# Performance work log

Hardware: AMD Instinct MI355X
Metric: run time of the kernel (lower is better)

## Reference

```python
import jax, jax.numpy as jnp
import numpy as np
from jax import lax

K = 15            # contrast_kernel
BRIGHT_T = 0.7    # brightness_threshold

def _box_filter(x, k):
    # x: [B,1,H,W]; uniform k x k conv with SAME (zero) padding, matching F.conv2d(padding=k//2)
    kernel = jnp.full((1, 1, k, k), 1.0 / (k * k), dtype=x.dtype)
    pad = k // 2
    return lax.conv_general_dilated(
        x, kernel, window_strides=(1, 1), padding=[(pad, pad), (pad, pad)],
        dimension_numbers=('NCHW', 'OIHW', 'NCHW'))

def _avg_pool_5x5(x):
    # avg_pool2d(kernel=5, stride=1, padding=2), count_include_pad=True (torch default)
    s = lax.reduce_window(x, jnp.array(0.0, x.dtype), lax.add,
                          window_dimensions=(1, 1, 5, 5), window_strides=(1, 1, 1, 1),
                          padding=[(0, 0), (0, 0), (2, 2), (2, 2)])
    return s / jnp.array(25.0, x.dtype)

def setup_inputs() -> dict:
    key = jax.random.key(0)
    img = jax.random.uniform(key, (16, 3, 1024, 1024), dtype=jnp.float32)
    return {"img": img}

def reference(img) -> jnp.ndarray:
    # luminance: [B,1,H,W]
    lum = (0.299 * img[:, 0:1] + 0.587 * img[:, 1:2] + 0.114 * img[:, 2:3])
    brightness_mask = jax.nn.sigmoid((lum - BRIGHT_T) * 10.0)
    local_mean = _box_filter(lum, K)
    local_var = _box_filter((lum - local_mean) ** 2, K)
    contrast_mask = jax.nn.sigmoid(local_var * 50.0 - 0.5)
    max_rgb = jnp.max(img, axis=1, keepdims=True)
    min_rgb = jnp.min(img, axis=1, keepdims=True)
    saturation = (max_rgb - min_rgb) / (max_rgb + 1e-8)
    low_sat_mask = jax.nn.sigmoid((0.3 - saturation) * 10.0)
    combined = jnp.clip(brightness_mask + 0.5 * contrast_mask * low_sat_mask, 0.0, 1.0)
    return _avg_pool_5x5(combined)
```

## Files before the change

### kernel.cpp

```cpp
#include <hip/hip_runtime.h>


#define BLOCK 512
typedef unsigned short u16;
typedef unsigned int u32;
typedef __attribute__((ext_vector_type(2))) float f32x2;

#define SL 104
#define S1 88

__device__ __forceinline__ float blo(u32 u){ return __uint_as_float(u << 16); }
__device__ __forceinline__ float bhi(u32 u){ return __uint_as_float(u & 0xffff0000u); }
__device__ __forceinline__ u32 pk2(float lo, float hi){
    u32 r; asm("v_cvt_pk_bf16_f32 %0, %1, %2" : "=v"(r) : "v"(lo), "v"(hi)); return r;
}
__device__ __forceinline__ f32x2 pka(f32x2 a, f32x2 b){
    f32x2 d; asm("v_pk_add_f32 %0, %1, %2" : "=v"(d) : "v"(a), "v"(b)); return d;
}
__device__ __forceinline__ f32x2 up2(u32 u){
    f32x2 r; r.x = __uint_as_float(u << 16); r.y = __uint_as_float(u & 0xffff0000u); return r;
}
__device__ __forceinline__ float sigf(float x){ return 1.f / (1.f + __expf(-x)); }
__device__ __forceinline__ float clamp01(float x){ return fminf(fmaxf(x, 0.f), 1.f); }
__device__ __forceinline__ void unp8(uint4 v, float* o){
    o[0]=blo(v.x); o[1]=bhi(v.x); o[2]=blo(v.y); o[3]=bhi(v.y);
    o[4]=blo(v.z); o[5]=bhi(v.z); o[6]=blo(v.w); o[7]=bhi(v.w);
}
__device__ __forceinline__ float satm(float r_, float g_, float b_){
    float mx = fmaxf(r_, fmaxf(g_, b_));
    float mn = fminf(r_, fminf(g_, b_));
    float sat = (mx - mn) / (mx + 1e-8f);
    return sigf((0.3f - sat) * 10.f);
}

template<bool EDGE>
__device__ __forceinline__ void body(const float* __restrict__ pR,
                                     const float* __restrict__ pG,
                                     const float* __restrict__ pB,
                                     float* __restrict__ po,
                                     int oy, int ox, int tid,
                                     u16* sLum, u16* sT1, u16* sDC)
{
    const float C225 = 1.f / 225.f;
    const float CF   = 50.f / 225.f;

    for (int task = tid; task < 96 * 6; task += BLOCK) {
        int r = task / 6, c = task - r * 6;
        int gy = oy - 16 + r;
        int gxb = ox - 16 + 16 * c;
        u32 pk[8];
        #pragma unroll
        for (int sq = 0; sq < 4; ++sq) {
            int gx = gxb + 4 * sq;
            float l0 = 0.f, l1 = 0.f, l2 = 0.f, l3 = 0.f;
            if (!EDGE || ((unsigned)gy < 1024u && (unsigned)gx < 1024u)) {
                int idx = gy * 1024 + gx;
                float4 R  = *(const float4*)&pR[idx];
                float4 G  = *(const float4*)&pG[idx];
                float4 Bc = *(const float4*)&pB[idx];
                l0 = fmaf(0.299f, R.x, fmaf(0.587f, G.x, 0.114f * Bc.x));
                l1 = fmaf(0.299f, R.y, fmaf(0.587f, G.y, 0.114f * Bc.y));
                l2 = fmaf(0.299f, R.z, fmaf(0.587f, G.z, 0.114f * Bc.z));
                l3 = fmaf(0.299f, R.w, fmaf(0.587f, G.w, 0.114f * Bc.w));
            }
            pk[2 * sq]     = pk2(l0, l1);
            pk[2 * sq + 1] = pk2(l2, l3);
        }
        u16* dst = &sLum[r * SL + 16 * c];
        *(uint4*)dst     = make_uint4(pk[0], pk[1], pk[2], pk[3]);
        *(uint4*)(dst+8) = make_uint4(pk[4], pk[5], pk[6], pk[7]);
    }
    __syncthreads();

    for (int task = tid; task < 6 * 96; task += BLOCK) {
        int g = task / 96, r = task - g * 96;
        int s0 = 16 * g;
        const u16* lr = &sLum[r * SL + s0];
        float lv[32];
        unp8(*(const uint4*)lr,        lv);
        unp8(*(const uint4*)(lr + 8),  lv + 8);
        unp8(*(const uint4*)(lr + 16), lv + 16);
        unp8(*(const uint4*)(lr + 24), lv + 24);
        float o[16];
        float s = 0.f;
        #pragma unroll
        for (int k = 0; k < 15; ++k) s += lv[k];
        o[0] = s;
        #pragma unroll
        for (int j = 1; j < 16; ++j) { s += lv[j + 14] - lv[j - 1]; o[j] = s; }
        u16* dst = &sT1[r * S1 + s0];
        if (g < 5) {
            *(uint4*)dst     = make_uint4(pk2(o[0],o[1]), pk2(o[2],o[3]),
                                          pk2(o[4],o[5]), pk2(o[6],o[7]));
            *(uint4*)(dst+8) = make_uint4(pk2(o[8],o[9]),  pk2(o[10],o[11]),
                                          pk2(o[12],o[13]),pk2(o[14],o[15]));
        } else {
            *(uint2*)dst = make_uint2(pk2(o[0],o[1]), pk2(o[2],o[3]));
        }
    }
    __syncthreads();

    for (int task = tid; task < 231; task += BLOCK) {
        int rg = task / 11, cg = task - rg * 11;
        int r0 = 4 * rg, c0 = 8 * cg;
        const u16* hp = &sT1[r0 * S1 + c0];
        f32x2 cs0, cs1, cs2, cs3;
        f32x2 n00,n01,n02,n03, n10,n11,n12,n13, n20,n21,n22,n23;
        {
            uint4 v = *(const uint4*)hp;
            cs0 = up2(v.x); cs1 = up2(v.y); cs2 = up2(v.z); cs3 = up2(v.w);
            n00 = -cs0; n01 = -cs1; n02 = -cs2; n03 = -cs3;
        }
        {
            uint4 v = *(const uint4*)(hp + S1);
            f32x2 e0 = up2(v.x), e1 = up2(v.y), e2 = up2(v.z), e3 = up2(v.w);
            n10 = -e0; n11 = -e1; n12 = -e2; n13 = -e3;
            cs0 = pka(cs0, e0); cs1 = pka(cs1, e1);
            cs2 = pka(cs2, e2); cs3 = pka(cs3, e3);
        }
        {
            uint4 v = *(const uint4*)(hp + 2 * S1);
            f32x2 e0 = up2(v.x), e1 = up2(v.y), e2 = up2(v.z), e3 = up2(v.w);
            n20 = -e0; n21 = -e1; n22 = -e2; n23 = -e3;
            cs0 = pka(cs0, e0); cs1 = pka(cs1, e1);
            cs2 = pka(cs2, e2); cs3 = pka(cs3, e3);
        }
        #pragma unroll
        for (int k = 3; k < 15; ++k) {
            uint4 v = *(const uint4*)(hp + k * S1);
            cs0 = pka(cs0, up2(v.x)); cs1 = pka(cs1, up2(v.y));
            cs2 = pka(cs2, up2(v.z)); cs3 = pka(cs3, up2(v.w));
        }
        auto emitD = [&](int row) {
            const u16* lrow = &sLum[(row + 7) * SL + c0];
            u32 aw  = *(const u32*)(lrow + 6);
            uint4 bv = *(const uint4*)(lrow + 8);
            float L0 = bhi(aw);
            float L1 = blo(bv.x), L2 = bhi(bv.x);
            float L3 = blo(bv.y), L4 = bhi(bv.y);
            float L5 = blo(bv.z), L6 = bhi(bv.z);
            float L7 = blo(bv.w);
            float t0 = fmaf(-C225, cs0.x, L0), t1 = fmaf(-C225, cs0.y, L1);
            float t2 = fmaf(-C225, cs1.x, L2), t3 = fmaf(-C225, cs1.y, L3);
            float t4 = fmaf(-C225, cs2.x, L4), t5 = fmaf(-C225, cs2.y, L5);
            float t6 = fmaf(-C225, cs3.x, L6), t7 = fmaf(-C225, cs3.y, L7);
            float d0=t0*t0, d1=t1*t1, d2=t2*t2, d3=t3*t3;
            float d4=t4*t4, d5=t5*t5, d6=t6*t6, d7=t7*t7;
            if (EDGE) {
                int gy = oy - 9 + row, gx = ox - 9 + c0;
                bool vy = (unsigned)gy < 1024u;
                d0 = (vy && (unsigned)(gx    ) < 1024u) ? d0 : 0.f;
                d1 = (vy && (unsigned)(gx + 1) < 1024u) ? d1 : 0.f;
                d2 = (vy && (unsigned)(gx + 2) < 1024u) ? d2 : 0.f;
                d3 = (vy && (unsigned)(gx + 3) < 1024u) ? d3 : 0.f;
                d4 = (vy && (unsigned)(gx + 4) < 1024u) ? d4 : 0.f;
                d5 = (vy && (unsigned)(gx + 5) < 1024u) ? d5 : 0.f;
                d6 = (vy && (unsigned)(gx + 6) < 1024u) ? d6 : 0.f;
                d7 = (vy && (unsigned)(gx + 7) < 1024u) ? d7 : 0.f;
            }
            *(uint4*)&sDC[row * S1 + c0] =
                make_uint4(pk2(d0,d1), pk2(d2,d3), pk2(d4,d5), pk2(d6,d7));
        };
        emitD(r0);
        {
            uint4 v = *(const uint4*)(hp + 15 * S1);
            cs0 = pka(pka(cs0, up2(v.x)), n00); cs1 = pka(pka(cs1, up2(v.y)), n01);
            cs2 = pka(pka(cs2, up2(v.z)), n02); cs3 = pka(pka(cs3, up2(v.w)), n03);
        }
        emitD(r0 + 1);
        {
            uint4 v = *(const uint4*)(hp + 16 * S1);
            cs0 = pka(pka(cs0, up2(v.x)), n10); cs1 = pka(pka(cs1, up2(v.y)), n11);
            cs2 = pka(pka(cs2, up2(v.z)), n12); cs3 = pka(pka(cs3, up2(v.w)), n13);
        }
        emitD(r0 + 2);
        {
            uint4 v = *(const uint4*)(hp + 17 * S1);
            cs0 = pka(pka(cs0, up2(v.x)), n20); cs1 = pka(pka(cs1, up2(v.y)), n21);
            cs2 = pka(pka(cs2, up2(v.z)), n22); cs3 = pka(pka(cs3, up2(v.w)), n23);
        }
        emitD(r0 + 3);
    }
    __syncthreads();

    for (int task = tid; task < 5 * 82; task += BLOCK) {
        int g = task / 82, r = task - g * 82;
        int s0 = 16 * g;
        const u16* dr = &sDC[r * S1 + s0];
        float lv[32];
        unp8(*(const uint4*)dr,        lv);
        unp8(*(const uint4*)(dr + 8),  lv + 8);
        unp8(*(const uint4*)(dr + 16), lv + 16);
        unp8(*(const uint4*)(dr + 24), lv + 24);
        float o[16];
        float s = 0.f;
        #pragma unroll
        for (int k = 0; k < 15; ++k) s += lv[k];
        o[0] = s;
        #pragma unroll
        for (int j = 1; j < 16; ++j) { s += lv[j + 14] - lv[j - 1]; o[j] = s; }
        u16* dst = &sT1[r * S1 + s0];
        if (g < 4) {
            *(uint4*)dst     = make_uint4(pk2(o[0],o[1]), pk2(o[2],o[3]),
                                          pk2(o[4],o[5]), pk2(o[6],o[7]));
            *(uint4*)(dst+8) = make_uint4(pk2(o[8],o[9]),  pk2(o[10],o[11]),
                                          pk2(o[12],o[13]),pk2(o[14],o[15]));
        } else {
            *(uint2*)dst = make_uint2(pk2(o[0],o[1]), pk2(o[2],o[3]));
        }
    }
    __syncthreads();

    for (int task = tid; task < 289; task += BLOCK) {
        int rg = task / 17, q = task - rg * 17;
        int r0 = 4 * rg, c0 = 4 * q;
        const u16* hp = &sT1[r0 * S1 + c0];
        f32x2 cs0, cs1, n00,n01, n10,n11, n20,n21;
        {
            uint2 v = *(const uint2*)hp;
            cs0 = up2(v.x); cs1 = up2(v.y);
            n00 = -cs0; n01 = -cs1;
        }
        {
            uint2 v = *(const uint2*)(hp + S1);
            f32x2 e0 = up2(v.x), e1 = up2(v.y);
            n10 = -e0; n11 = -e1;
            cs0 = pka(cs0, e0); cs1 = pka(cs1, e1);
        }
        {
            uint2 v = *(const uint2*)(hp + 2 * S1);
            f32x2 e0 = up2(v.x), e1 = up2(v.y);
            n20 = -e0; n21 = -e1;
            cs0 = pka(cs0, e0); cs1 = pka(cs1, e1);
        }
        #pragma unroll
        for (int k = 3; k < 15; ++k) {
            uint2 v = *(const uint2*)(hp + k * S1);
            cs0 = pka(cs0, up2(v.x)); cs1 = pka(cs1, up2(v.y));
        }
        auto emitC = [&](int row) {
            float cm0 = sigf(fmaf(cs0.x, CF, -0.5f));
            float cm1 = sigf(fmaf(cs0.y, CF, -0.5f));
            float cm2 = sigf(fmaf(cs1.x, CF, -0.5f));
            float cm3 = sigf(fmaf(cs1.y, CF, -0.5f));
            const u16* lr = &sLum[(row + 14) * SL + c0 + 14];
            u32 la = *(const u32*)lr;
            u32 lb = *(const u32*)(lr + 2);
            float bm0 = sigf((blo(la) - 0.7f) * 10.f);
            float bm1 = sigf((bhi(la) - 0.7f) * 10.f);
            float bm2 = sigf((blo(lb) - 0.7f) * 10.f);
            float bm3 = sigf((bhi(lb) - 0.7f) * 10.f);
            int gy = oy - 2 + row, gx0 = ox - 2 + c0;
            int i0 = gy * 1024 + gx0;
            float2 z2 = make_float2(0.f, 0.f);
            float2 Ra, Rb, Ga, Gb, Ba, Bb;
            bool va = true, vb = true;
            if (EDGE) {
                bool vy = (unsigned)gy < 1024u;
                va = vy && (unsigned)gx0 < 1024u;
                vb = vy && (unsigned)(gx0 + 2) < 1024u;
                Ra = va ? *(const float2*)&pR[i0]     : z2;
                Rb = vb ? *(const float2*)&pR[i0 + 2] : z2;
                Ga = va ? *(const float2*)&pG[i0]     : z2;
                Gb = vb ? *(const float2*)&pG[i0 + 2] : z2;
                Ba = va ? *(const float2*)&pB[i0]     : z2;
                Bb = vb ? *(const float2*)&pB[i0 + 2] : z2;
            } else {
                Ra = *(const float2*)&pR[i0];  Rb = *(const float2*)&pR[i0 + 2];
                Ga = *(const float2*)&pG[i0];  Gb = *(const float2*)&pG[i0 + 2];
                Ba = *(const float2*)&pB[i0];  Bb = *(const float2*)&pB[i0 + 2];
            }
            float cb0 = clamp01(bm0 + 0.5f * cm0 * satm(Ra.x, Ga.x, Ba.x));
            float cb1 = clamp01(bm1 + 0.5f * cm1 * satm(Ra.y, Ga.y, Ba.y));
            float cb2 = clamp01(bm2 + 0.5f * cm2 * satm(Rb.x, Gb.x, Bb.x));
            float cb3 = clamp01(bm3 + 0.5f * cm3 * satm(Rb.y, Gb.y, Bb.y));
            if (EDGE) {
                cb0 = va ? cb0 : 0.f;  cb1 = va ? cb1 : 0.f;
                cb2 = vb ? cb2 : 0.f;  cb3 = vb ? cb3 : 0.f;
            }
            *(uint2*)&sDC[row * S1 + c0] = make_uint2(pk2(cb0,cb1), pk2(cb2,cb3));
        };
        emitC(r0);
        {
            uint2 v = *(const uint2*)(hp + 15 * S1);
            cs0 = pka(pka(cs0, up2(v.x)), n00); cs1 = pka(pka(cs1, up2(v.y)), n01);
        }
        emitC(r0 + 1);
        {
            uint2 v = *(const uint2*)(hp + 16 * S1);
            cs0 = pka(pka(cs0, up2(v.x)), n10); cs1 = pka(pka(cs1, up2(v.y)), n11);
        }
        emitC(r0 + 2);
        {
            uint2 v = *(const uint2*)(hp + 17 * S1);
            cs0 = pka(pka(cs0, up2(v.x)), n20); cs1 = pka(pka(cs1, up2(v.y)), n21);
        }
        emitC(r0 + 3);
    }
    __syncthreads();

    for (int task = tid; task < 4 * 68; task += BLOCK) {
        int g = task / 68, r = task - g * 68;
        int s0 = 16 * g;
        const u16* cr = &sDC[r * S1 + s0];
        float cv[24];
        unp8(*(const uint4*)cr,        cv);
        unp8(*(const uint4*)(cr + 8),  cv + 8);
        unp8(*(const uint4*)(cr + 16), cv + 16);
        float o[16];
        float s = cv[0] + cv[1] + cv[2] + cv[3] + cv[4];
        o[0] = s;
        #pragma unroll
        for (int j = 1; j < 16; ++j) { s += cv[j + 4] - cv[j - 1]; o[j] = s; }
        u16* dst = &sT1[r * S1 + s0];
        *(uint4*)dst = make_uint4(pk2(o[0], o[1]), pk2(o[2], o[3]),
                                  pk2(o[4], o[5]), pk2(o[6], o[7]));
        *(uint4*)(dst + 8) = make_uint4(pk2(o[8],  o[9]),  pk2(o[10], o[11]),
                                        pk2(o[12], o[13]), pk2(o[14], o[15]));
    }
    __syncthreads();

    for (int task = tid; task < 256; task += BLOCK) {
        int rg = task >> 4, q = task & 15;
        int r0 = 4 * rg, c0 = 4 * q;
        const u16* hp = &sT1[r0 * S1 + c0];
        f32x2 cs0, cs1, n00,n01, n10,n11, n20,n21;
        {
            uint2 v = *(const uint2*)hp;
            cs0 = up2(v.x); cs1 = up2(v.y);
            n00 = -cs0; n01 = -cs1;
        }
        {
            uint2 v = *(const uint2*)(hp + S1);
            f32x2 e0 = up2(v.x), e1 = up2(v.y);
            n10 = -e0; n11 = -e1;
            cs0 = pka(cs0, e0); cs1 = pka(cs1, e1);
        }
        {
            uint2 v = *(const uint2*)(hp + 2 * S1);
            f32x2 e0 = up2(v.x), e1 = up2(v.y);
            n20 = -e0; n21 = -e1;
            cs0 = pka(cs0, e0); cs1 = pka(cs1, e1);
        }
        {
            uint2 v = *(const uint2*)(hp + 3 * S1);
            cs0 = pka(cs0, up2(v.x)); cs1 = pka(cs1, up2(v.y));
        }
        {
            uint2 v = *(const uint2*)(hp + 4 * S1);
            cs0 = pka(cs0, up2(v.x)); cs1 = pka(cs1, up2(v.y));
        }
        const float C25 = 1.f / 25.f;
        float* o0 = po + (size_t)(oy + r0) * 1024 + ox + c0;
        *(float4*)o0 = make_float4(cs0.x*C25, cs0.y*C25, cs1.x*C25, cs1.y*C25);
        {
            uint2 v = *(const uint2*)(hp + 5 * S1);
            cs0 = pka(pka(cs0, up2(v.x)), n00); cs1 = pka(pka(cs1, up2(v.y)), n01);
        }
        *(float4*)(o0 + 1024) = make_float4(cs0.x*C25, cs0.y*C25, cs1.x*C25, cs1.y*C25);
        {
            uint2 v = *(const uint2*)(hp + 6 * S1);
            cs0 = pka(pka(cs0, up2(v.x)), n10); cs1 = pka(pka(cs1, up2(v.y)), n11);
        }
        *(float4*)(o0 + 2048) = make_float4(cs0.x*C25, cs0.y*C25, cs1.x*C25, cs1.y*C25);
        {
            uint2 v = *(const uint2*)(hp + 7 * S1);
            cs0 = pka(pka(cs0, up2(v.x)), n20); cs1 = pka(pka(cs1, up2(v.y)), n21);
        }
        *(float4*)(o0 + 3072) = make_float4(cs0.x*C25, cs0.y*C25, cs1.x*C25, cs1.y*C25);
    }
}

__global__ __launch_bounds__(BLOCK, 6)
void wrd_kernel(const float* __restrict__ img, float* __restrict__ out) {
    __shared__ u16 sLum[96 * SL + 16];
    __shared__ u16 sT1[98 * S1];
    __shared__ u16 sDC[84 * S1 + 16];

    int bid = blockIdx.x, nwg = gridDim.x;
    int flat = ((nwg & 7) == 0) ? ((bid & 7) * (nwg >> 3) + (bid >> 3)) : bid;
    const int b = flat >> 8;
    const int t = flat & 255;
    const int oy = (t >> 4) * 64, ox = (t & 15) * 64;

    const float* pR = img + (size_t)b * 3145728u;
    const float* pG = pR + 1048576;
    const float* pB = pR + 2097152;
    float* po = out + (size_t)b * 1048576u;

    bool edge = (ox == 0) | (oy == 0) | (ox == 960) | (oy == 960);
    if (edge) body<true >(pR, pG, pB, po, oy, ox, threadIdx.x, sLum, sT1, sDC);
    else      body<false>(pR, pG, pB, po, oy, ox, threadIdx.x, sLum, sT1, sDC);
}

extern "C" void kernel_launch(void* const* d_in, const int* in_sizes, int n_in,
                              void* d_out, int out_size, void* d_ws, size_t ws_size,
                              hipStream_t stream) {
    const float* img = (const float*)d_in[0];
    float* out = (float*)d_out;
    int Bn = in_sizes[0] / (3 * 1024 * 1024);
    int nwg = Bn * 256;
    hipLaunchKernelGGL(wrd_kernel, dim3(nwg), dim3(BLOCK), 0, stream, img, out);
}
```

Baseline: 116.1 us.

## Split vertical passes into 2-row tasks and reorder horizontal task mapping

The vertical box-sum passes now handle 2 output rows per task instead of 4, sharing one partial column sum. This roughly doubles the task count, so more of the 512 threads have work, at the cost of recomputing overlapping column sums. The horizontal passes change task indexing to be row-major (row outer, segment inner), which alters LDS bank access patterns across lanes. The shared sT1 buffer shrinks slightly.

```diff
diff --git a/kernel.cpp b/kernel.cpp
--- a/kernel.cpp
+++ b/kernel.cpp
@@ -72,8 +72,8 @@
     }
     __syncthreads();
 
-    for (int task = tid; task < 6 * 96; task += BLOCK) {
-        int g = task / 96, r = task - g * 96;
+    for (int task = tid; task < 96 * 6; task += BLOCK) {
+        int r = task / 6, g = task - r * 6;
         int s0 = 16 * g;
         const u16* lr = &sLum[r * SL + s0];
         float lv[32];
@@ -100,38 +100,26 @@
     }
     __syncthreads();
 
-    for (int task = tid; task < 231; task += BLOCK) {
+    for (int task = tid; task < 451; task += BLOCK) {
         int rg = task / 11, cg = task - rg * 11;
-        int r0 = 4 * rg, c0 = 8 * cg;
+        int r0 = 2 * rg, c0 = 8 * cg;
         const u16* hp = &sT1[r0 * S1 + c0];
-        f32x2 cs0, cs1, cs2, cs3;
-        f32x2 n00,n01,n02,n03, n10,n11,n12,n13, n20,n21,n22,n23;
+        f32x2 a0, a1, a2, a3, cs0, cs1, cs2, cs3;
         {
             uint4 v = *(const uint4*)hp;
+            a0 = up2(v.x); a1 = up2(v.y); a2 = up2(v.z); a3 = up2(v.w);
+        }
+        {
+            uint4 v = *(const uint4*)(hp + S1);
             cs0 = up2(v.x); cs1 = up2(v.y); cs2 = up2(v.z); cs3 = up2(v.w);
-            n00 = -cs0; n01 = -cs1; n02 = -cs2; n03 = -cs3;
-        }
-        {
-            uint4 v = *(const uint4*)(hp + S1);
-            f32x2 e0 = up2(v.x), e1 = up2(v.y), e2 = up2(v.z), e3 = up2(v.w);
-            n10 = -e0; n11 = -e1; n12 = -e2; n13 = -e3;
-            cs0 = pka(cs0, e0); cs1 = pka(cs1, e1);
-            cs2 = pka(cs2, e2); cs3 = pka(cs3, e3);
-        }
-        {
-            uint4 v = *(const uint4*)(hp + 2 * S1);
-            f32x2 e0 = up2(v.x), e1 = up2(v.y), e2 = up2(v.z), e3 = up2(v.w);
-            n20 = -e0; n21 = -e1; n22 = -e2; n23 = -e3;
-            cs0 = pka(cs0, e0); cs1 = pka(cs1, e1);
-            cs2 = pka(cs2, e2); cs3 = pka(cs3, e3);
-        }
-        #pragma unroll
-        for (int k = 3; k < 15; ++k) {
+        }
+        #pragma unroll
+        for (int k = 2; k <= 14; ++k) {
             uint4 v = *(const uint4*)(hp + k * S1);
             cs0 = pka(cs0, up2(v.x)); cs1 = pka(cs1, up2(v.y));
             cs2 = pka(cs2, up2(v.z)); cs3 = pka(cs3, up2(v.w));
         }
-        auto emitD = [&](int row) {
+        auto emitD = [&](int row, f32x2 t0, f32x2 t1, f32x2 t2, f32x2 t3) {
             const u16* lrow = &sLum[(row + 7) * SL + c0];
             u32 aw  = *(const u32*)(lrow + 6);
             uint4 bv = *(const uint4*)(lrow + 8);
@@ -140,12 +128,12 @@
             float L3 = blo(bv.y), L4 = bhi(bv.y);
             float L5 = blo(bv.z), L6 = bhi(bv.z);
             float L7 = blo(bv.w);
-            float t0 = fmaf(-C225, cs0.x, L0), t1 = fmaf(-C225, cs0.y, L1);
-            float t2 = fmaf(-C225, cs1.x, L2), t3 = fmaf(-C225, cs1.y, L3);
-            float t4 = fmaf(-C225, cs2.x, L4), t5 = fmaf(-C225, cs2.y, L5);
-            float t6 = fmaf(-C225, cs3.x, L6), t7 = fmaf(-C225, cs3.y, L7);
-            float d0=t0*t0, d1=t1*t1, d2=t2*t2, d3=t3*t3;
-            float d4=t4*t4, d5=t5*t5, d6=t6*t6, d7=t7*t7;
+            float t_0 = fmaf(-C225, t0.x, L0), t_1 = fmaf(-C225, t0.y, L1);
+            float t_2 = fmaf(-C225, t1.x, L2), t_3 = fmaf(-C225, t1.y, L3);
+            float t_4 = fmaf(-C225, t2.x, L4), t_5 = fmaf(-C225, t2.y, L5);
+            float t_6 = fmaf(-C225, t3.x, L6), t_7 = fmaf(-C225, t3.y, L7);
+            float d0=t_0*t_0, d1=t_1*t_1, d2=t_2*t_2, d3=t_3*t_3;
+            float d4=t_4*t_4, d5=t_5*t_5, d6=t_6*t_6, d7=t_7*t_7;
             if (EDGE) {
                 int gy = oy - 9 + row, gx = ox - 9 + c0;
                 bool vy = (unsigned)gy < 1024u;
@@ -161,30 +149,17 @@
             *(uint4*)&sDC[row * S1 + c0] =
                 make_uint4(pk2(d0,d1), pk2(d2,d3), pk2(d4,d5), pk2(d6,d7));
         };
-        emitD(r0);
+        emitD(r0, pka(cs0,a0), pka(cs1,a1), pka(cs2,a2), pka(cs3,a3));
         {
             uint4 v = *(const uint4*)(hp + 15 * S1);
-            cs0 = pka(pka(cs0, up2(v.x)), n00); cs1 = pka(pka(cs1, up2(v.y)), n01);
-            cs2 = pka(pka(cs2, up2(v.z)), n02); cs3 = pka(pka(cs3, up2(v.w)), n03);
-        }
-        emitD(r0 + 1);
-        {
-            uint4 v = *(const uint4*)(hp + 16 * S1);
-            cs0 = pka(pka(cs0, up2(v.x)), n10); cs1 = pka(pka(cs1, up2(v.y)), n11);
-            cs2 = pka(pka(cs2, up2(v.z)), n12); cs3 = pka(pka(cs3, up2(v.w)), n13);
-        }
-        emitD(r0 + 2);
-        {
-            uint4 v = *(const uint4*)(hp + 17 * S1);
-            cs0 = pka(pka(cs0, up2(v.x)), n20); cs1 = pka(pka(cs1, up2(v.y)), n21);
-            cs2 = pka(pka(cs2, up2(v.z)), n22); cs3 = pka(pka(cs3, up2(v.w)), n23);
-        }
-        emitD(r0 + 3);
-    }
-    __syncthreads();
-
-    for (int task = tid; task < 5 * 82; task += BLOCK) {
-        int g = task / 82, r = task - g * 82;
+            emitD(r0 + 1, pka(cs0, up2(v.x)), pka(cs1, up2(v.y)),
+                          pka(cs2, up2(v.z)), pka(cs3, up2(v.w)));
+        }
+    }
+    __syncthreads();
+
+    for (int task = tid; task < 82 * 5; task += BLOCK) {
+        int r = task / 5, g = task - r * 5;
         int s0 = 16 * g;
         const u16* dr = &sDC[r * S1 + s0];
         float lv[32];
@@ -299,8 +274,8 @@
     }
     __syncthreads();
 
-    for (int task = tid; task < 4 * 68; task += BLOCK) {
-        int g = task / 68, r = task - g * 68;
+    for (int task = tid; task < 68 * 4; task += BLOCK) {
+        int r = task >> 2, g = task & 3;
         int s0 = 16 * g;
         const u16* cr = &sDC[r * S1 + s0];
         float cv[24];
@@ -320,27 +295,22 @@
     }
     __syncthreads();
 
-    for (int task = tid; task < 256; task += BLOCK) {
+    for (int task = tid; task < 512; task += BLOCK) {
         int rg = task >> 4, q = task & 15;
-        int r0 = 4 * rg, c0 = 4 * q;
+        int r0 = 2 * rg, c0 = 4 * q;
         const u16* hp = &sT1[r0 * S1 + c0];
-        f32x2 cs0, cs1, n00,n01, n10,n11, n20,n21;
+        f32x2 a0, a1, cs0, cs1;
         {
             uint2 v = *(const uint2*)hp;
+            a0 = up2(v.x); a1 = up2(v.y);
+        }
+        {
+            uint2 v = *(const uint2*)(hp + S1);
             cs0 = up2(v.x); cs1 = up2(v.y);
-            n00 = -cs0; n01 = -cs1;
-        }
-        {
-            uint2 v = *(const uint2*)(hp + S1);
-            f32x2 e0 = up2(v.x), e1 = up2(v.y);
-            n10 = -e0; n11 = -e1;
-            cs0 = pka(cs0, e0); cs1 = pka(cs1, e1);
         }
         {
             uint2 v = *(const uint2*)(hp + 2 * S1);
-            f32x2 e0 = up2(v.x), e1 = up2(v.y);
-            n20 = -e0; n21 = -e1;
-            cs0 = pka(cs0, e0); cs1 = pka(cs1, e1);
+            cs0 = pka(cs0, up2(v.x)); cs1 = pka(cs1, up2(v.y));
         }
         {
             uint2 v = *(const uint2*)(hp + 3 * S1);
@@ -352,29 +322,20 @@
         }
         const float C25 = 1.f / 25.f;
         float* o0 = po + (size_t)(oy + r0) * 1024 + ox + c0;
-        *(float4*)o0 = make_float4(cs0.x*C25, cs0.y*C25, cs1.x*C25, cs1.y*C25);
+        f32x2 t0 = pka(cs0, a0), t1 = pka(cs1, a1);
+        *(float4*)o0 = make_float4(t0.x*C25, t0.y*C25, t1.x*C25, t1.y*C25);
         {
             uint2 v = *(const uint2*)(hp + 5 * S1);
-            cs0 = pka(pka(cs0, up2(v.x)), n00); cs1 = pka(pka(cs1, up2(v.y)), n01);
-        }
-        *(float4*)(o0 + 1024) = make_float4(cs0.x*C25, cs0.y*C25, cs1.x*C25, cs1.y*C25);
-        {
-            uint2 v = *(const uint2*)(hp + 6 * S1);
-            cs0 = pka(pka(cs0, up2(v.x)), n10); cs1 = pka(pka(cs1, up2(v.y)), n11);
-        }
-        *(float4*)(o0 + 2048) = make_float4(cs0.x*C25, cs0.y*C25, cs1.x*C25, cs1.y*C25);
-        {
-            uint2 v = *(const uint2*)(hp + 7 * S1);
-            cs0 = pka(pka(cs0, up2(v.x)), n20); cs1 = pka(pka(cs1, up2(v.y)), n21);
-        }
-        *(float4*)(o0 + 3072) = make_float4(cs0.x*C25, cs0.y*C25, cs1.x*C25, cs1.y*C25);
+            t0 = pka(cs0, up2(v.x)); t1 = pka(cs1, up2(v.y));
+        }
+        *(float4*)(o0 + 1024) = make_float4(t0.x*C25, t0.y*C25, t1.x*C25, t1.y*C25);
     }
 }
 
 __global__ __launch_bounds__(BLOCK, 6)
 void wrd_kernel(const float* __restrict__ img, float* __restrict__ out) {
     __shared__ u16 sLum[96 * SL + 16];
-    __shared__ u16 sT1[98 * S1];
+    __shared__ u16 sT1[96 * S1];
     __shared__ u16 sDC[84 * S1 + 16];
 
     int bid = blockIdx.x, nwg = gridDim.x;
```

After: 120.1 us. +3.4%, slower.
